# Optimization experiments

Hardware: AMD Instinct MI355X
Metric: run time of the kernel (lower is better)

Reference implementation:

```python
import jax, jax.numpy as jnp
import numpy as np

B, INPUT_DIM, N_CAT, D_LAT, N_Q, N_HID = 4096, 3072, 1024, 256, 32, 4096


def _lin_init(k, fan_in, fan_out):
    kw, _ = jax.random.split(k)
    w = jax.random.normal(kw, (fan_out, fan_in), jnp.float32) / jnp.sqrt(jnp.float32(fan_in))
    b = jnp.zeros((fan_out,), jnp.float32)
    return w, b


def setup_inputs() -> dict:
    key = jax.random.key(0)
    ks = jax.random.split(key, 8)
    x = jax.random.uniform(ks[0], (B, INPUT_DIM), jnp.float32)
    embed_pool = jax.random.normal(ks[1], (N_CAT, D_LAT), jnp.float32)
    ew1, eb1 = _lin_init(ks[2], INPUT_DIM, N_HID)
    ew2, eb2 = _lin_init(ks[3], N_HID, N_HID)
    ew3, eb3 = _lin_init(ks[4], N_HID, N_Q * D_LAT)
    dw1, db1 = _lin_init(ks[5], N_Q * D_LAT, N_HID)
    dw2, db2 = _lin_init(ks[6], N_HID, N_HID)
    dw3, db3 = _lin_init(ks[7], N_HID, INPUT_DIM)
    return {"x": x, "embed_pool": embed_pool,
            "ew1": ew1, "eb1": eb1, "ew2": ew2, "eb2": eb2, "ew3": ew3, "eb3": eb3,
            "dw1": dw1, "db1": db1, "dw2": dw2, "db2": db2, "dw3": dw3, "db3": db3}


def _gelu(h):
    return jax.nn.gelu(h, approximate=False)  # torch nn.GELU default (erf)


def reference(x, embed_pool, ew1, eb1, ew2, eb2, ew3, eb3,
              dw1, db1, dw2, db2, dw3, db3):
    sg = jax.lax.stop_gradient
    # encoder (dropout inactive at eval)
    h = _gelu(x @ ew1.T + eb1)
    h = _gelu(h @ ew2.T + eb2)
    z_e = (h @ ew3.T + eb3).reshape(B, N_Q, D_LAT)           # [B, n_query, d]
    # codebook dot-product scoring + argmax (no grad)
    factor = jnp.einsum('cd,bnd->bnc', sg(embed_pool), sg(z_e))  # [B, n, c]
    z_index = jnp.argmax(factor, axis=2)                      # [B, n]
    z_discrete = jax.nn.one_hot(z_index, N_CAT, dtype=jnp.int32)
    z_q = embed_pool[z_index]                                 # gather [B, n, d]
    # straight-through
    z_ss = (z_e - sg(z_e) + sg(z_q)).reshape(B, N_Q * D_LAT)
    # decoder
    g = _gelu(z_ss @ dw1.T + db1)
    g = _gelu(g @ dw2.T + db2)
    x_pred = jax.nn.sigmoid(g @ dw3.T + db3)
    loss = jnp.mean((x - x_pred) ** 2)
    loss = loss + jnp.mean((sg(z_e) - z_q) ** 2)
    loss = loss + 0.25 * jnp.mean((z_e - sg(z_q)) ** 2)
    loss = loss / x.shape[0]
    return (x_pred, z_discrete, loss)
```

## Files before the change

### kernel.cpp

```cpp
#include <hip/hip_runtime.h>
#include <math.h>


typedef __attribute__((ext_vector_type(8))) short  bf16x8;
typedef __attribute__((ext_vector_type(4))) float  f32x4;

__device__ __forceinline__ unsigned short bf16_rne(float f) {
    unsigned int u = __float_as_uint(f);
    u += 0x7FFFu + ((u >> 16) & 1u);
    return (unsigned short)(u >> 16);
}
__device__ __forceinline__ float bf16_tof(unsigned short h) {
    return __uint_as_float(((unsigned int)h) << 16);
}

__device__ __forceinline__ void gload16(const void* g, void* l) {
    __builtin_amdgcn_global_load_lds(
        (const __attribute__((address_space(1))) void*)g,
        (__attribute__((address_space(3))) void*)l, 16, 0, 0);
}

#define BM 128
#define BN 128
#define BK 16

template<int ACT>
__global__ __launch_bounds__(256) void gemm_nt(
    const float* __restrict__ A, const float* __restrict__ Bw,
    const float* __restrict__ bias, float* __restrict__ C,
    int M, int N, int K)
{
    __shared__ float As[BK][BM + 4];
    __shared__ float Bs[BK][BN + 4];

    const int tid = threadIdx.x;
    const int tx = tid & 15;
    const int ty = tid >> 4;
    const int m0 = blockIdx.y * BM;
    const int n0 = blockIdx.x * BN;
    const int lr = tid >> 2;
    const int lk = (tid & 3) << 2;

    float acc[8][8];
    #pragma unroll
    for (int i = 0; i < 8; ++i)
        #pragma unroll
        for (int j = 0; j < 8; ++j) acc[i][j] = 0.0f;

    const float* Ap = A + (size_t)(m0 + lr) * K + lk;
    const float* Bp = Bw + (size_t)(n0 + lr) * K + lk;
    const size_t strideR = (size_t)64 * K;

    for (int k0 = 0; k0 < K; k0 += BK) {
        float4 a0 = *(const float4*)(Ap + k0);
        float4 a1 = *(const float4*)(Ap + k0 + strideR);
        float4 b0 = *(const float4*)(Bp + k0);
        float4 b1 = *(const float4*)(Bp + k0 + strideR);
        __syncthreads();
        As[lk+0][lr]    = a0.x; As[lk+1][lr]    = a0.y; As[lk+2][lr]    = a0.z; As[lk+3][lr]    = a0.w;
        As[lk+0][lr+64] = a1.x; As[lk+1][lr+64] = a1.y; As[lk+2][lr+64] = a1.z; As[lk+3][lr+64] = a1.w;
        Bs[lk+0][lr]    = b0.x; Bs[lk+1][lr]    = b0.y; Bs[lk+2][lr]    = b0.z; Bs[lk+3][lr]    = b0.w;
        Bs[lk+0][lr+64] = b1.x; Bs[lk+1][lr+64] = b1.y; Bs[lk+2][lr+64] = b1.z; Bs[lk+3][lr+64] = b1.w;
        __syncthreads();
        #pragma unroll
        for (int kk = 0; kk < BK; ++kk) {
            float a_[8], b_[8];
            *(float4*)&a_[0] = *(const float4*)&As[kk][ty * 4];
            *(float4*)&a_[4] = *(const float4*)&As[kk][ty * 4 + 64];
            *(float4*)&b_[0] = *(const float4*)&Bs[kk][tx * 4];
            *(float4*)&b_[4] = *(const float4*)&Bs[kk][tx * 4 + 64];
            #pragma unroll
            for (int i = 0; i < 8; ++i)
                #pragma unroll
                for (int j = 0; j < 8; ++j)
                    acc[i][j] = fmaf(a_[i], b_[j], acc[i][j]);
        }
    }

    float bv[8];
    *(float4*)&bv[0] = *(const float4*)&bias[n0 + tx * 4];
    *(float4*)&bv[4] = *(const float4*)&bias[n0 + 64 + tx * 4];

    #pragma unroll
    for (int i = 0; i < 8; ++i) {
        const int rbase = (i < 4) ? (ty * 4 + i) : (64 + ty * 4 + (i - 4));
        const size_t row = (size_t)(m0 + rbase);
        float out[8];
        #pragma unroll
        for (int j = 0; j < 8; ++j) {
            float v = acc[i][j] + bv[j];
            if (ACT == 1) v = 0.5f * v * (1.0f + erff(v * 0.70710678118654752440f));
            out[j] = v;
        }
        float* cp0 = C + row * N + n0 + tx * 4;
        float* cp1 = C + row * N + n0 + 64 + tx * 4;
        *(float4*)cp0 = *(const float4*)&out[0];
        *(float4*)cp1 = *(const float4*)&out[4];
    }
}

__global__ __launch_bounds__(256) void split_bf16_2(
    const float* __restrict__ in, unsigned short* __restrict__ o0,
    unsigned short* __restrict__ o1, int n4)
{
    int i = blockIdx.x * 256 + threadIdx.x;
    if (i >= n4) return;
    float4 v = ((const float4*)in)[i];
    ushort4 a, b;
    float* vp = (float*)&v;
    unsigned short* ap = (unsigned short*)&a;
    unsigned short* bp = (unsigned short*)&b;
    #pragma unroll
    for (int k = 0; k < 4; ++k) {
        float x = vp[k];
        unsigned short h0 = bf16_rne(x);
        float r = x - bf16_tof(h0);
        ap[k] = h0; bp[k] = bf16_rne(r);
    }
    ((ushort4*)o0)[i] = a;
    ((ushort4*)o1)[i] = b;
}

template<int ACT, int OUT>
__global__ __launch_bounds__(256) void gemm_split(
    const unsigned short* __restrict__ A0, const unsigned short* __restrict__ A1,
    const unsigned short* __restrict__ B0, const unsigned short* __restrict__ B1,
    const float* __restrict__ bias,
    float* __restrict__ Cf,
    unsigned short* __restrict__ C0, unsigned short* __restrict__ C1,
    int M, int N, int K,
    const float* __restrict__ Xref, float* __restrict__ sse_acc)
{
    __shared__ unsigned short As[128 * 64];
    __shared__ unsigned short Bs[128 * 64];
    __shared__ float red[4];

    const int tid  = threadIdx.x;
    const int lane = tid & 63;
    const int wid  = tid >> 6;
    const int wm   = wid >> 1;
    const int wn   = wid & 1;
    const int m0   = blockIdx.y * 128;
    const int n0   = blockIdx.x * 128;

    const int sr  = tid >> 3;
    const int scb = ((tid & 7) << 4) ^ ((sr & 7) << 4);

    const int l15  = lane & 15;
    const int xorr = (lane & 7) << 4;
    const int ksl0 = (((lane >> 4) << 4)     ) ^ xorr;
    const int ksl1 = (((lane >> 4) << 4) + 64) ^ xorr;

    f32x4 acc[4][4];
    const f32x4 fzero = {0.0f, 0.0f, 0.0f, 0.0f};
    #pragma unroll
    for (int i = 0; i < 4; ++i)
        #pragma unroll
        for (int j = 0; j < 4; ++j) acc[i][j] = fzero;

    #pragma unroll 1
    for (int ia = 0; ia < 2; ++ia) {
        #pragma unroll 1
        for (int ib = 0; ia + ib < 2; ++ib) {
            const unsigned short* Ap = (ia == 0) ? A0 : A1;
            const unsigned short* Bp = (ib == 0) ? B0 : B1;
            #pragma unroll 1
            for (int k0 = 0; k0 < K; k0 += 64) {
                __syncthreads();
                #pragma unroll
                for (int it = 0; it < 4; ++it) {
                    gload16((const char*)(Ap + (size_t)(m0 + it * 32 + sr) * K + k0) + scb,
                            (char*)As + it * 4096 + tid * 16);
                    gload16((const char*)(Bp + (size_t)(n0 + it * 32 + sr) * K + k0) + scb,
                            (char*)Bs + it * 4096 + tid * 16);
                }
                __syncthreads();
                #pragma unroll
                for (int kb = 0; kb < 2; ++kb) {
                    const int ks = kb ? ksl1 : ksl0;
                    bf16x8 av[4], bv[4];
                    #pragma unroll
                    for (int i = 0; i < 4; ++i) {
                        av[i] = *(const bf16x8*)((const char*)As + (wm * 64 + i * 16 + l15) * 128 + ks);
                        bv[i] = *(const bf16x8*)((const char*)Bs + (wn * 64 + i * 16 + l15) * 128 + ks);
                    }
                    #pragma unroll
                    for (int i = 0; i < 4; ++i)
                        #pragma unroll
                        for (int j = 0; j < 4; ++j)
                            acc[i][j] = __builtin_amdgcn_mfma_f32_16x16x32_bf16(
                                av[i], bv[j], acc[i][j], 0, 0, 0);
                }
            }
        }
    }

    float bj[4];
    #pragma unroll
    for (int j = 0; j < 4; ++j) bj[j] = bias[n0 + wn * 64 + j * 16 + l15];

    float sse_local = 0.0f;
    const int r4 = (lane >> 4) << 2;
    #pragma unroll
    for (int i = 0; i < 4; ++i) {
        #pragma unroll
        for (int v = 0; v < 4; ++v) {
            const size_t m = (size_t)(m0 + wm * 64 + i * 16 + r4 + v);
            #pragma unroll
            for (int j = 0; j < 4; ++j) {
                const size_t n = (size_t)(n0 + wn * 64 + j * 16 + l15);
                float val = acc[i][j][v] + bj[j];
                if (ACT == 1)      val = 0.5f * val * (1.0f + erff(val * 0.70710678118654752440f));
                else if (ACT == 2) val = 1.0f / (1.0f + expf(-val));
                const size_t off = m * (size_t)N + n;
                if (OUT == 0) {
                    Cf[off] = val;
                    if (ACT == 2) {
                        float d = Xref[off] - val;
                        sse_local = fmaf(d, d, sse_local);
                    }
                } else {
                    unsigned short h0 = bf16_rne(val);
                    float r = val - bf16_tof(h0);
                    C0[off] = h0; C1[off] = bf16_rne(r);
                }
            }
        }
    }

    if (ACT == 2) {
        #pragma unroll
        for (int off = 32; off > 0; off >>= 1) sse_local += __shfl_down(sse_local, off);
        if (lane == 0) red[wid] = sse_local;
        __syncthreads();
        if (tid == 0) atomicAdd(sse_acc, red[0] + red[1] + red[2] + red[3]);
    }
}

__global__ __launch_bounds__(256) void score_argmax(
    const float* __restrict__ Z, const float* __restrict__ E,
    int* __restrict__ idx_out)
{
    __shared__ float As[BK][BM + 4];
    __shared__ float Bs[BK][BN + 4];
    __shared__ float rv[BM][17];
    __shared__ int   ri[BM][17];

    const int tid = threadIdx.x;
    const int tx = tid & 15;
    const int ty = tid >> 4;
    const int m0 = blockIdx.x * BM;
    const int lr = tid >> 2;
    const int lk = (tid & 3) << 2;

    const float* Ap = Z + (size_t)(m0 + lr) * 256 + lk;

    float best[8]; int besti[8];
    #pragma unroll
    for (int i = 0; i < 8; ++i) { best[i] = -3.4e38f; besti[i] = 0; }

    for (int c0 = 0; c0 < 1024; c0 += BN) {
        float acc[8][8];
        #pragma unroll
        for (int i = 0; i < 8; ++i)
            #pragma unroll
            for (int j = 0; j < 8; ++j) acc[i][j] = 0.0f;

        const float* Bp = E + (size_t)(c0 + lr) * 256 + lk;
        for (int k0 = 0; k0 < 256; k0 += BK) {
            float4 a0 = *(const float4*)(Ap + k0);
            float4 a1 = *(const float4*)(Ap + k0 + (size_t)64 * 256);
            float4 b0 = *(const float4*)(Bp + k0);
            float4 b1 = *(const float4*)(Bp + k0 + (size_t)64 * 256);
            __syncthreads();
            As[lk+0][lr]    = a0.x; As[lk+1][lr]    = a0.y; As[lk+2][lr]    = a0.z; As[lk+3][lr]    = a0.w;
            As[lk+0][lr+64] = a1.x; As[lk+1][lr+64] = a1.y; As[lk+2][lr+64] = a1.z; As[lk+3][lr+64] = a1.w;
            Bs[lk+0][lr]    = b0.x; Bs[lk+1][lr]    = b0.y; Bs[lk+2][lr]    = b0.z; Bs[lk+3][lr]    = b0.w;
            Bs[lk+0][lr+64] = b1.x; Bs[lk+1][lr+64] = b1.y; Bs[lk+2][lr+64] = b1.z; Bs[lk+3][lr+64] = b1.w;
            __syncthreads();
            #pragma unroll
            for (int kk = 0; kk < BK; ++kk) {
                float a_[8], b_[8];
                *(float4*)&a_[0] = *(const float4*)&As[kk][ty * 8];
                *(float4*)&a_[4] = *(const float4*)&As[kk][ty * 8 + 4];
                *(float4*)&b_[0] = *(const float4*)&Bs[kk][tx * 8];
                *(float4*)&b_[4] = *(const float4*)&Bs[kk][tx * 8 + 4];
                #pragma unroll
                for (int i = 0; i < 8; ++i)
                    #pragma unroll
                    for (int j = 0; j < 8; ++j)
                        acc[i][j] = fmaf(a_[i], b_[j], acc[i][j]);
            }
        }
        #pragma unroll
        for (int j = 0; j < 8; ++j) {
            const int col = c0 + tx * 8 + j;
            #pragma unroll
            for (int i = 0; i < 8; ++i) {
                if (acc[i][j] > best[i]) { best[i] = acc[i][j]; besti[i] = col; }
            }
        }
    }

    #pragma unroll
    for (int i = 0; i < 8; ++i) { rv[ty * 8 + i][tx] = best[i]; ri[ty * 8 + i][tx] = besti[i]; }
    __syncthreads();
    if (tid < BM) {
        float bvv = rv[tid][0]; int bii = ri[tid][0];
        #pragma unroll
        for (int t = 1; t < 16; ++t) {
            float v = rv[tid][t]; int ii = ri[tid][t];
            if (v > bvv || (v == bvv && ii < bii)) { bvv = v; bii = ii; }
        }
        idx_out[m0 + tid] = bii;
    }
}

__global__ __launch_bounds__(256) void gather_zq(
    const float* __restrict__ Z, const float* __restrict__ E,
    const unsigned short* __restrict__ E0, const unsigned short* __restrict__ E1,
    const int* __restrict__ idx,
    unsigned short* __restrict__ Zq0, unsigned short* __restrict__ Zq1,
    float* __restrict__ onehot, float* __restrict__ acc)
{
    __shared__ float red[4];
    const size_t g = (size_t)blockIdx.x * 256 + threadIdx.x;
    const int q = (int)(g >> 8);
    const int d = (int)(g & 255);
    const int c = idx[q];
    const size_t eoff = (size_t)c * 256 + d;
    const float e = E[eoff];
    const float z = Z[g];
    Zq0[g] = E0[eoff];
    Zq1[g] = E1[eoff];
    if (d == 0) onehot[(size_t)q * 1024 + c] = 1.0f;
    float v = (z - e) * (z - e);
    #pragma unroll
    for (int off = 32; off > 0; off >>= 1) v += __shfl_down(v, off);
    if ((threadIdx.x & 63) == 0) red[threadIdx.x >> 6] = v;
    __syncthreads();
    if (threadIdx.x == 0) atomicAdd(acc + 1, red[0] + red[1] + red[2] + red[3]);
}

__global__ void finalize_loss(const float* __restrict__ acc, float* __restrict__ out)
{
    const float m1 = acc[0] * (1.0f / (4096.0f * 3072.0f));
    const float m2 = acc[1] * (1.0f / (4096.0f * 32.0f * 256.0f));
    out[0] = (m1 + 1.25f * m2) * (1.0f / 4096.0f);
}

extern "C" void kernel_launch(void* const* d_in, const int* in_sizes, int n_in,
                              void* d_out, int out_size, void* d_ws, size_t ws_size,
                              hipStream_t stream)
{
    const float* x   = (const float*)d_in[0];
    const float* E   = (const float*)d_in[1];
    const float* ew1 = (const float*)d_in[2];
    const float* eb1 = (const float*)d_in[3];
    const float* ew2 = (const float*)d_in[4];
    const float* eb2 = (const float*)d_in[5];
    const float* ew3 = (const float*)d_in[6];
    const float* eb3 = (const float*)d_in[7];
    const float* dw1 = (const float*)d_in[8];
    const float* db1 = (const float*)d_in[9];
    const float* dw2 = (const float*)d_in[10];
    const float* db2 = (const float*)d_in[11];
    const float* dw3 = (const float*)d_in[12];
    const float* db3 = (const float*)d_in[13];

    float* outf   = (float*)d_out;
    float* xpred  = outf;
    float* onehot = outf + (size_t)4096 * 3072;
    float* loss   = onehot + (size_t)4096 * 32 * 1024;

    char* oh = (char*)onehot;
    float* H1 = (float*)(oh);
    float* H2 = (float*)(oh + 67108864);

    char* ws = (char*)d_ws;
    float*          ZE  = (float*)(ws);
    unsigned short* V0  = (unsigned short*)(ws);
    unsigned short* V1  = (unsigned short*)(ws + 67108864);
    unsigned short* ZQ0 = (unsigned short*)(ws + 134217728);
    unsigned short* ZQ1 = (unsigned short*)(ws + 201326592);
    unsigned short* G10 = (unsigned short*)(ws + 268435456);
    unsigned short* G11 = (unsigned short*)(ws + 301989888);
    unsigned short* G20 = (unsigned short*)(ws + 335544320);
    unsigned short* G21 = (unsigned short*)(ws + 369098752);
    unsigned short* E0  = (unsigned short*)(ws + 402653184);
    unsigned short* E1  = (unsigned short*)(ws + 403177472);
    int*   IDX = (int*)  (ws + 403701760);
    float* ACC = (float*)(ws + 404226048);

    dim3 blk(256);

    gemm_nt<1><<<dim3(32, 32), blk, 0, stream>>>(x,  ew1, eb1, H1, 4096, 4096, 3072);
    gemm_nt<1><<<dim3(32, 32), blk, 0, stream>>>(H1, ew2, eb2, H2, 4096, 4096, 4096);
    gemm_nt<0><<<dim3(64, 32), blk, 0, stream>>>(H2, ew3, eb3, ZE, 4096, 8192, 4096);

    score_argmax<<<dim3(1024), blk, 0, stream>>>(ZE, E, IDX);

    hipMemsetAsync(ACC, 0, 2 * sizeof(float), stream);
    hipMemsetAsync(onehot, 0, (size_t)4096 * 32 * 1024 * sizeof(float), stream);

    split_bf16_2<<<256, blk, 0, stream>>>(E, E0, E1, 65536);
    gather_zq<<<dim3(131072), blk, 0, stream>>>(ZE, E, E0, E1, IDX, ZQ0, ZQ1, onehot, ACC);

    split_bf16_2<<<32768, blk, 0, stream>>>(dw1, V0, V1, 8388608);
    gemm_split<1,2><<<dim3(32, 32), blk, 0, stream>>>(ZQ0, ZQ1, V0, V1, db1,
        nullptr, G10, G11, 4096, 4096, 8192, nullptr, nullptr);
    split_bf16_2<<<16384, blk, 0, stream>>>(dw2, V0, V1, 4194304);
    gemm_split<1,2><<<dim3(32, 32), blk, 0, stream>>>(G10, G11, V0, V1, db2,
        nullptr, G20, G21, 4096, 4096, 4096, nullptr, nullptr);
    split_bf16_2<<<12288, blk, 0, stream>>>(dw3, V0, V1, 3145728);
    gemm_split<2,0><<<dim3(24, 32), blk, 0, stream>>>(G20, G21, V0, V1, db3,
        xpred, nullptr, nullptr, 4096, 3072, 4096, x, ACC);

    finalize_loss<<<1, 1, 0, stream>>>(ACC, loss);
}
```

Baseline: 11.18 ms.

## Fuse split-bf16 GEMM passes into one K loop and widen fp32 GEMM K tile

The split-bf16 GEMM used to make three separate passes over K (hi*hi, hi*lo, lo*hi), reloading tiles each time. It now stages all four hi/lo A and B tiles per K step and issues the three MFMAs together, so each K step needs one load phase and one pair of barriers instead of three. The fp32 GEMM's K tile grows from 16 to 32, and both kernels get a minimum-occupancy launch bound of two blocks. The costs are doubled LDS use and higher register pressure in the split kernel. The launch bound may also force register spills.

```diff
diff --git a/kernel.cpp b/kernel.cpp
--- a/kernel.cpp
+++ b/kernel.cpp
@@ -23,15 +23,16 @@
 #define BM 128
 #define BN 128
 #define BK 16
+#define BK2 32
 
 template<int ACT>
-__global__ __launch_bounds__(256) void gemm_nt(
+__global__ __launch_bounds__(256, 2) void gemm_nt(
     const float* __restrict__ A, const float* __restrict__ Bw,
     const float* __restrict__ bias, float* __restrict__ C,
     int M, int N, int K)
 {
-    __shared__ float As[BK][BM + 4];
-    __shared__ float Bs[BK][BN + 4];
+    __shared__ float As[BK2][BM + 4];
+    __shared__ float Bs[BK2][BN + 4];
 
     const int tid = threadIdx.x;
     const int tx = tid & 15;
@@ -51,19 +52,27 @@
     const float* Bp = Bw + (size_t)(n0 + lr) * K + lk;
     const size_t strideR = (size_t)64 * K;
 
-    for (int k0 = 0; k0 < K; k0 += BK) {
-        float4 a0 = *(const float4*)(Ap + k0);
-        float4 a1 = *(const float4*)(Ap + k0 + strideR);
-        float4 b0 = *(const float4*)(Bp + k0);
-        float4 b1 = *(const float4*)(Bp + k0 + strideR);
+    for (int k0 = 0; k0 < K; k0 += BK2) {
+        float4 a00 = *(const float4*)(Ap + k0);
+        float4 a01 = *(const float4*)(Ap + k0 + 16);
+        float4 a10 = *(const float4*)(Ap + k0 + strideR);
+        float4 a11 = *(const float4*)(Ap + k0 + strideR + 16);
+        float4 b00 = *(const float4*)(Bp + k0);
+        float4 b01 = *(const float4*)(Bp + k0 + 16);
+        float4 b10 = *(const float4*)(Bp + k0 + strideR);
+        float4 b11 = *(const float4*)(Bp + k0 + strideR + 16);
         __syncthreads();
-        As[lk+0][lr]    = a0.x; As[lk+1][lr]    = a0.y; As[lk+2][lr]    = a0.z; As[lk+3][lr]    = a0.w;
-        As[lk+0][lr+64] = a1.x; As[lk+1][lr+64] = a1.y; As[lk+2][lr+64] = a1.z; As[lk+3][lr+64] = a1.w;
-        Bs[lk+0][lr]    = b0.x; Bs[lk+1][lr]    = b0.y; Bs[lk+2][lr]    = b0.z; Bs[lk+3][lr]    = b0.w;
-        Bs[lk+0][lr+64] = b1.x; Bs[lk+1][lr+64] = b1.y; Bs[lk+2][lr+64] = b1.z; Bs[lk+3][lr+64] = b1.w;
+        As[lk+0][lr]     = a00.x; As[lk+1][lr]     = a00.y; As[lk+2][lr]     = a00.z; As[lk+3][lr]     = a00.w;
+        As[lk+16][lr]    = a01.x; As[lk+17][lr]    = a01.y; As[lk+18][lr]    = a01.z; As[lk+19][lr]    = a01.w;
+        As[lk+0][lr+64]  = a10.x; As[lk+1][lr+64]  = a10.y; As[lk+2][lr+64]  = a10.z; As[lk+3][lr+64]  = a10.w;
+        As[lk+16][lr+64] = a11.x; As[lk+17][lr+64] = a11.y; As[lk+18][lr+64] = a11.z; As[lk+19][lr+64] = a11.w;
+        Bs[lk+0][lr]     = b00.x; Bs[lk+1][lr]     = b00.y; Bs[lk+2][lr]     = b00.z; Bs[lk+3][lr]     = b00.w;
+        Bs[lk+16][lr]    = b01.x; Bs[lk+17][lr]    = b01.y; Bs[lk+18][lr]    = b01.z; Bs[lk+19][lr]    = b01.w;
+        Bs[lk+0][lr+64]  = b10.x; Bs[lk+1][lr+64]  = b10.y; Bs[lk+2][lr+64]  = b10.z; Bs[lk+3][lr+64]  = b10.w;
+        Bs[lk+16][lr+64] = b11.x; Bs[lk+17][lr+64] = b11.y; Bs[lk+18][lr+64] = b11.z; Bs[lk+19][lr+64] = b11.w;
         __syncthreads();
         #pragma unroll
-        for (int kk = 0; kk < BK; ++kk) {
+        for (int kk = 0; kk < BK2; ++kk) {
             float a_[8], b_[8];
             *(float4*)&a_[0] = *(const float4*)&As[kk][ty * 4];
             *(float4*)&a_[4] = *(const float4*)&As[kk][ty * 4 + 64];
@@ -122,7 +131,7 @@
 }
 
 template<int ACT, int OUT>
-__global__ __launch_bounds__(256) void gemm_split(
+__global__ __launch_bounds__(256, 2) void gemm_split(
     const unsigned short* __restrict__ A0, const unsigned short* __restrict__ A1,
     const unsigned short* __restrict__ B0, const unsigned short* __restrict__ B1,
     const float* __restrict__ bias,
@@ -131,8 +140,10 @@
     int M, int N, int K,
     const float* __restrict__ Xref, float* __restrict__ sse_acc)
 {
-    __shared__ unsigned short As[128 * 64];
-    __shared__ unsigned short Bs[128 * 64];
+    __shared__ unsigned short As0[128 * 64];
+    __shared__ unsigned short As1[128 * 64];
+    __shared__ unsigned short Bs0[128 * 64];
+    __shared__ unsigned short Bs1[128 * 64];
     __shared__ float red[4];
 
     const int tid  = threadIdx.x;
@@ -159,39 +170,40 @@
         for (int j = 0; j < 4; ++j) acc[i][j] = fzero;
 
     #pragma unroll 1
-    for (int ia = 0; ia < 2; ++ia) {
-        #pragma unroll 1
-        for (int ib = 0; ia + ib < 2; ++ib) {
-            const unsigned short* Ap = (ia == 0) ? A0 : A1;
-            const unsigned short* Bp = (ib == 0) ? B0 : B1;
-            #pragma unroll 1
-            for (int k0 = 0; k0 < K; k0 += 64) {
-                __syncthreads();
+    for (int k0 = 0; k0 < K; k0 += 64) {
+        __syncthreads();
+        #pragma unroll
+        for (int it = 0; it < 4; ++it) {
+            const size_t go = (size_t)(m0 + it * 32 + sr) * K + k0;
+            const size_t ho = (size_t)(n0 + it * 32 + sr) * K + k0;
+            const int lo = it * 4096 + tid * 16;
+            gload16((const char*)(A0 + go) + scb, (char*)As0 + lo);
+            gload16((const char*)(A1 + go) + scb, (char*)As1 + lo);
+            gload16((const char*)(B0 + ho) + scb, (char*)Bs0 + lo);
+            gload16((const char*)(B1 + ho) + scb, (char*)Bs1 + lo);
+        }
+        __syncthreads();
+        #pragma unroll
+        for (int kb = 0; kb < 2; ++kb) {
+            const int ks = kb ? ksl1 : ksl0;
+            bf16x8 av0[4], av1[4], bv0[4], bv1[4];
+            #pragma unroll
+            for (int i = 0; i < 4; ++i) {
+                const int ra = (wm * 64 + i * 16 + l15) * 128 + ks;
+                const int rb = (wn * 64 + i * 16 + l15) * 128 + ks;
+                av0[i] = *(const bf16x8*)((const char*)As0 + ra);
+                av1[i] = *(const bf16x8*)((const char*)As1 + ra);
+                bv0[i] = *(const bf16x8*)((const char*)Bs0 + rb);
+                bv1[i] = *(const bf16x8*)((const char*)Bs1 + rb);
+            }
+            #pragma unroll
+            for (int i = 0; i < 4; ++i)
                 #pragma unroll
-                for (int it = 0; it < 4; ++it) {
-                    gload16((const char*)(Ap + (size_t)(m0 + it * 32 + sr) * K + k0) + scb,
-                            (char*)As + it * 4096 + tid * 16);
-                    gload16((const char*)(Bp + (size_t)(n0 + it * 32 + sr) * K + k0) + scb,
-                            (char*)Bs + it * 4096 + tid * 16);
+                for (int j = 0; j < 4; ++j) {
+                    acc[i][j] = __builtin_amdgcn_mfma_f32_16x16x32_bf16(av0[i], bv0[j], acc[i][j], 0, 0, 0);
+                    acc[i][j] = __builtin_amdgcn_mfma_f32_16x16x32_bf16(av0[i], bv1[j], acc[i][j], 0, 0, 0);
+                    acc[i][j] = __builtin_amdgcn_mfma_f32_16x16x32_bf16(av1[i], bv0[j], acc[i][j], 0, 0, 0);
                 }
-                __syncthreads();
-                #pragma unroll
-                for (int kb = 0; kb < 2; ++kb) {
-                    const int ks = kb ? ksl1 : ksl0;
-                    bf16x8 av[4], bv[4];
-                    #pragma unroll
-                    for (int i = 0; i < 4; ++i) {
-                        av[i] = *(const bf16x8*)((const char*)As + (wm * 64 + i * 16 + l15) * 128 + ks);
-                        bv[i] = *(const bf16x8*)((const char*)Bs + (wn * 64 + i * 16 + l15) * 128 + ks);
-                    }
-                    #pragma unroll
-                    for (int i = 0; i < 4; ++i)
-                        #pragma unroll
-                        for (int j = 0; j < 4; ++j)
-                            acc[i][j] = __builtin_amdgcn_mfma_f32_16x16x32_bf16(
-                                av[i], bv[j], acc[i][j], 0, 0, 0);
-                }
-            }
         }
     }
 
```

Result: faster. 10.79 ms (-3.5%).
